# Performance work log

Hardware: AMD Instinct MI355X
Metric: run time of the kernel (lower is better)

The kernel has to match this reference:

```python
import jax, jax.numpy as jnp
import numpy as np


def setup_inputs() -> dict:
    key = jax.random.key(0)
    k1, k2, k3, k4, k5 = jax.random.split(key, 5)
    B, N, M, D = 4096, 2048, 2048, 9
    return {
        "x": jax.random.normal(k1, (B, N), dtype=jnp.float32),
        "eternal_weights": jax.random.normal(k2, (D, N, M), dtype=jnp.float32),
        "eternal_biases": jax.random.normal(k3, (M,), dtype=jnp.float32),
        "classical_weights": jax.random.normal(k4, (N, M), dtype=jnp.float32),
        "classical_biases": jax.random.normal(k5, (M,), dtype=jnp.float32),
    }


def _eternal_probs(eternal_weights, n, m):
    # The gate matrix is cos*I - sin*P + sin*P^T with P the circular shift,
    # so (gate @ s)[i] = cos*s[i] - sin*s[(i+1)%n] + sin*s[(i-1)%n].
    # Vectorize over all m output units at once: state is [m, n].
    state0 = jnp.full((m, n), 1.0 / np.sqrt(n), dtype=eternal_weights.dtype)
    angles = eternal_weights[:, :m, :3]  # [D, m, 3] -- weights[depth, j, 0/1/2]

    def gate(state, angle):  # angle: [m]
        c = jnp.cos(angle)[:, None]
        s = jnp.sin(angle)[:, None]
        return c * state - s * jnp.roll(state, -1, axis=1) + s * jnp.roll(state, 1, axis=1)

    def step(state, ang):  # ang: [m, 3] -- consciousness, intelligence, wisdom
        state = gate(state, ang[:, 0])
        state = gate(state, ang[:, 1])
        state = gate(state, ang[:, 2])
        return state, None

    state, _ = jax.lax.scan(step, state0, angles)
    return jnp.abs(state[:, 0]) ** 2  # [m]


def reference(x, eternal_weights, eternal_biases, classical_weights, classical_biases):
    # eternal_biases exists as a parameter in the original module but is unused in forward.
    n = x.shape[1]
    m = classical_weights.shape[1]
    classical = x @ classical_weights + classical_biases  # [B, m]
    probs = _eternal_probs(eternal_weights, n, m)  # [m], identical for every batch row
    return jnp.tanh(classical + probs[None, :])
```

## Files before the change

### kernel.cpp

```cpp
#include <hip/hip_runtime.h>
#include <hip/hip_fp8.h>
#include <stdint.h>

static constexpr int MM = 4096;
static constexpr int KK = 2048;
static constexpr int NN = 2048;

typedef float floatx16 __attribute__((ext_vector_type(16)));
typedef __bf16 bf16x8 __attribute__((ext_vector_type(8)));
typedef unsigned short u16x8 __attribute__((ext_vector_type(8)));
typedef int intx4 __attribute__((ext_vector_type(4)));
typedef int intx8 __attribute__((ext_vector_type(8)));
typedef unsigned char u8x16 __attribute__((ext_vector_type(16)));

__device__ __forceinline__ unsigned short bf16_rne(float x) {
  union { float f; uint32_t u; } c; c.f = x;
  uint32_t u = c.u;
  u += 0x7fffu + ((u >> 16) & 1u);
  return (unsigned short)(u >> 16);
}
__device__ __forceinline__ float bf16_as_f32(unsigned short h) {
  union { float f; uint32_t u; } c; c.u = ((uint32_t)h) << 16;
  return c.f;
}
__device__ __forceinline__ unsigned char f32_to_e4m3(float x) {
  __hip_fp8_e4m3 q(x);
  return (unsigned char)q.__x;
}
__device__ __forceinline__ float fast_tanh(float x) {
  float e = __expf(2.0f * x);
  return 1.0f - 2.0f / (e + 1.0f);
}


__global__ __launch_bounds__(256) void prepass_kernel(
    const float* __restrict__ x, const float* __restrict__ E,
    const float* __restrict__ W, const float* __restrict__ cb,
    unsigned short* __restrict__ ahi, unsigned char* __restrict__ a8,
    unsigned char* __restrict__ al8,
    unsigned short* __restrict__ bhi, unsigned char* __restrict__ b8,
    unsigned char* __restrict__ bl8, float* __restrict__ bias2) {
  __shared__ float tile[64][65];
  const int blk = blockIdx.x;
  const int tid = threadIdx.x;

  if (blk < 2048) {
    int idx = blk * 256 + tid;
    int row = idx >> 7;
    int u = idx & 127;
    int g = u >> 2;
    int c4 = u & 3;
    const float4* s = (const float4*)(x + (size_t)row * KK + u * 16);
    float v[16];
#pragma unroll
    for (int q = 0; q < 4; q++) {
      float4 t = s[q];
      v[q * 4 + 0] = t.x; v[q * 4 + 1] = t.y; v[q * 4 + 2] = t.z; v[q * 4 + 3] = t.w;
    }
    unsigned short h[16];
    u8x16 f8, fl8;
#pragma unroll
    for (int e = 0; e < 16; e++) {
      h[e] = bf16_rne(v[e]);
      float lo = v[e] - bf16_as_f32(h[e]);
      f8[e] = f32_to_e4m3(v[e]);
      fl8[e] = f32_to_e4m3(lo * 512.0f);
    }
    size_t rb = (size_t)row * KK;
#pragma unroll
    for (int cc = 0; cc < 2; cc++) {
      int c8 = c4 * 2 + cc;
      int phys8 = (c8 + row + (row >> 3)) & 7;
      u16x8 o;
#pragma unroll
      for (int e = 0; e < 8; e++) o[e] = h[cc * 8 + e];
      *(u16x8*)(ahi + rb + g * 64 + phys8 * 8) = o;
    }
    int phys4 = (c4 + (row >> 1) + (row >> 3)) & 3;
    *(u8x16*)(a8 + rb + g * 64 + phys4 * 16) = f8;
    *(u8x16*)(al8 + rb + g * 64 + phys4 * 16) = fl8;
  } else if (blk < 3072) {
    const int wb = blk - 2048;
    const int n0 = (wb & 31) * 64;
    const int k0 = (wb >> 5) * 64;
#pragma unroll
    for (int i = 0; i < 4; i++) {
      int t = tid + i * 256;
      int kr = t >> 4;
      int nc = (t & 15) * 4;
      const float4 vv = *(const float4*)(W + (size_t)(k0 + kr) * NN + n0 + nc);
      tile[nc + 0][kr] = vv.x;
      tile[nc + 1][kr] = vv.y;
      tile[nc + 2][kr] = vv.z;
      tile[nc + 3][kr] = vv.w;
    }
    __syncthreads();
    const int nl = tid >> 2;
    const int q = tid & 3;
    const int n = n0 + nl;
    float v[16];
    unsigned short h[16];
    u8x16 f8, fl8;
#pragma unroll
    for (int e = 0; e < 16; e++) {
      v[e] = tile[nl][q * 16 + e];
      h[e] = bf16_rne(v[e]);
      float lo = v[e] - bf16_as_f32(h[e]);
      f8[e] = f32_to_e4m3(v[e]);
      fl8[e] = f32_to_e4m3(lo * 512.0f);
    }
    size_t rb = (size_t)n * KK + k0;
#pragma unroll
    for (int cc = 0; cc < 2; cc++) {
      int c8 = q * 2 + cc;
      int phys8 = (c8 + n + (n >> 3)) & 7;
      u16x8 o;
#pragma unroll
      for (int e = 0; e < 8; e++) o[e] = h[cc * 8 + e];
      *(u16x8*)(bhi + rb + phys8 * 8) = o;
    }
    int phys4 = (q + (n >> 1) + (n >> 3)) & 3;
    *(u8x16*)(b8 + rb + phys4 * 16) = f8;
    *(u8x16*)(bl8 + rb + phys4 * 16) = fl8;
  } else {
    int i = (blk - 3072) * 256 + tid;
    if (i < NN) {
      float p = 1.0f / 2048.0f;
#pragma unroll
      for (int d = 0; d < 9; d++) {
        const float4 a = *(const float4*)(E + (size_t)d * (2048 * 2048) + (size_t)i * 2048);
        float c0 = cosf(a.x), c1 = cosf(a.y), c2 = cosf(a.z);
        p *= (c0 * c0) * (c1 * c1) * (c2 * c2);
      }
      bias2[i] = cb[i] + p;
    }
  }
}

#define GLL(dst, src)                                                        \
  __builtin_amdgcn_global_load_lds(                                          \
      (const __attribute__((address_space(1))) void*)(src),                  \
      (__attribute__((address_space(3))) void*)(dst), 16, 0, 0)

__global__ __launch_bounds__(256, 2) void gemm_tanh_kernel(
    const unsigned short* __restrict__ Ahi, const unsigned char* __restrict__ A8,
    const unsigned char* __restrict__ Al8,
    const unsigned short* __restrict__ Bhi, const unsigned char* __restrict__ B8,
    const unsigned char* __restrict__ Bl8,
    const float* __restrict__ bias2, float* __restrict__ out) {
  __shared__ __align__(16) unsigned short sAh[128 * 64];
  __shared__ __align__(16) unsigned short sBh[128 * 64];
  __shared__ __align__(16) unsigned char sA8[128 * 64];
  __shared__ __align__(16) unsigned char sAl[128 * 64];
  __shared__ __align__(16) unsigned char sB8[128 * 64];
  __shared__ __align__(16) unsigned char sBl[128 * 64];

  const int tid = threadIdx.x;
  const int lane = tid & 63;
  const int wave = tid >> 6;
  const int wm = (wave >> 1) * 64;
  const int wn = (wave & 1) * 64;

  const int id = blockIdx.x;
  const int cid = id >> 4, lid = id & 15;
  const int bm = ((cid >> 2) * 4 + (lid >> 2)) * 128;
  const int bn = ((cid & 3) * 4 + (lid & 3)) * 128;

  const size_t a16 = (size_t)(bm + (tid >> 3)) * KK + (tid & 7) * 8;
  const size_t b16 = (size_t)(bn + (tid >> 3)) * KK + (tid & 7) * 8;
  const size_t a8b = (size_t)(bm + (tid >> 2)) * KK + (tid & 3) * 16;
  const size_t b8b = (size_t)(bn + (tid >> 2)) * KK + (tid & 3) * 16;
  const int lds16 = tid * 8;
  const int lds8 = tid * 16;

  const int r31 = lane & 31;
  const int half = lane >> 5;

  floatx16 acch[2][2], accc[2][2];
#pragma unroll
  for (int i = 0; i < 2; i++)
#pragma unroll
    for (int j = 0; j < 2; j++)
#pragma unroll
      for (int r = 0; r < 16; r++) { acch[i][j][r] = 0.f; accc[i][j][r] = 0.f; }

  for (int k0 = 0; k0 < KK; k0 += 64) {
#pragma unroll
    for (int p = 0; p < 4; p++) {
      const size_t go = k0 + (size_t)(32 * p) * KK;
      GLL(&sAh[p * 2048 + lds16], Ahi + a16 + go);
      GLL(&sBh[p * 2048 + lds16], Bhi + b16 + go);
    }
#pragma unroll
    for (int p = 0; p < 2; p++) {
      const size_t go = k0 + (size_t)(64 * p) * KK;
      GLL(&sA8[p * 4096 + lds8], A8 + a8b + go);
      GLL(&sAl[p * 4096 + lds8], Al8 + a8b + go);
      GLL(&sB8[p * 4096 + lds8], B8 + b8b + go);
      GLL(&sBl[p * 4096 + lds8], Bl8 + b8b + go);
    }
    __syncthreads();

#pragma unroll
    for (int s = 0; s < 4; s++) {
      const int c8 = s * 2 + half;
      bf16x8 fa[2], fb[2];
#pragma unroll
      for (int t = 0; t < 2; t++) {
        int rowA = wm + t * 32 + r31;
        int ao = rowA * 64 + ((c8 + rowA + (rowA >> 3)) & 7) * 8;
        fa[t] = *(const bf16x8*)(&sAh[ao]);
        int rowB = wn + t * 32 + r31;
        int bo = rowB * 64 + ((c8 + rowB + (rowB >> 3)) & 7) * 8;
        fb[t] = *(const bf16x8*)(&sBh[bo]);
      }
#pragma unroll
      for (int i = 0; i < 2; i++)
#pragma unroll
        for (int j = 0; j < 2; j++)
          acch[i][j] = __builtin_amdgcn_mfma_f32_32x32x16_bf16(fa[i], fb[j], acch[i][j], 0, 0, 0);
    }

    {
      intx8 fal[2], fb8[2];
#pragma unroll
      for (int t = 0; t < 2; t++) {
        int rowA = wm + t * 32 + r31;
        int rowB = wn + t * 32 + r31;
#pragma unroll
        for (int cc = 0; cc < 2; cc++) {
          int c4 = half * 2 + cc;
          int pa = (c4 + (rowA >> 1) + (rowA >> 3)) & 3;
          ((intx4*)&fal[t])[cc] = *(const intx4*)(&sAl[rowA * 64 + pa * 16]);
          int pb = (c4 + (rowB >> 1) + (rowB >> 3)) & 3;
          ((intx4*)&fb8[t])[cc] = *(const intx4*)(&sB8[rowB * 64 + pb * 16]);
        }
      }
#pragma unroll
      for (int i = 0; i < 2; i++)
#pragma unroll
        for (int j = 0; j < 2; j++)
          accc[i][j] = __builtin_amdgcn_mfma_scale_f32_32x32x64_f8f6f4(
              fal[i], fb8[j], accc[i][j], 0, 0, 0, 0x7f7f7f7f, 0, 0x7f7f7f7f);

      intx8 fa8[2], fbl[2];
#pragma unroll
      for (int t = 0; t < 2; t++) {
        int rowA = wm + t * 32 + r31;
        int rowB = wn + t * 32 + r31;
#pragma unroll
        for (int cc = 0; cc < 2; cc++) {
          int c4 = half * 2 + cc;
          int pa = (c4 + (rowA >> 1) + (rowA >> 3)) & 3;
          ((intx4*)&fa8[t])[cc] = *(const intx4*)(&sA8[rowA * 64 + pa * 16]);
          int pb = (c4 + (rowB >> 1) + (rowB >> 3)) & 3;
          ((intx4*)&fbl[t])[cc] = *(const intx4*)(&sBl[rowB * 64 + pb * 16]);
        }
      }
#pragma unroll
      for (int i = 0; i < 2; i++)
#pragma unroll
        for (int j = 0; j < 2; j++)
          accc[i][j] = __builtin_amdgcn_mfma_scale_f32_32x32x64_f8f6f4(
              fa8[i], fbl[j], accc[i][j], 0, 0, 0, 0x7f7f7f7f, 0, 0x7f7f7f7f);
    }
    __syncthreads();
  }

#pragma unroll
  for (int j = 0; j < 2; j++) {
    int col = bn + wn + j * 32 + r31;
    float b2 = bias2[col];
#pragma unroll
    for (int i = 0; i < 2; i++) {
      int row0 = bm + wm + i * 32 + 4 * half;
#pragma unroll
      for (int r = 0; r < 16; r++) {
        int row = row0 + (r & 3) + 8 * (r >> 2);
        float val = acch[i][j][r] + accc[i][j][r] * (1.0f / 512.0f) + b2;
        __builtin_nontemporal_store(fast_tanh(val), &out[(size_t)row * NN + col]);
      }
    }
  }
}

__global__ __launch_bounds__(256) void fallback_gemm(
    const float* __restrict__ x, const float* __restrict__ E,
    const float* __restrict__ W, const float* __restrict__ cb,
    float* __restrict__ out) {
  __shared__ float sA[16][16];
  __shared__ float sB[16][17];
  __shared__ float sbias[16];
  const int tx = threadIdx.x, ty = threadIdx.y;
  const int row = blockIdx.y * 16 + ty;
  const int col = blockIdx.x * 16 + tx;
  if (ty == 0) {
    float p = 1.0f / 2048.0f;
    for (int d = 0; d < 9; d++) {
      const float* a = E + (size_t)d * (2048 * 2048) + (size_t)col * 2048;
      for (int t = 0; t < 3; t++) { float c = cosf(a[t]); p *= c * c; }
    }
    sbias[tx] = p + cb[col];
  }
  float acc = 0.f;
  for (int k0 = 0; k0 < KK; k0 += 16) {
    __syncthreads();
    sA[ty][tx] = x[(size_t)row * KK + k0 + tx];
    sB[ty][tx] = W[(size_t)(k0 + ty) * NN + col];
    __syncthreads();
#pragma unroll
    for (int kk = 0; kk < 16; kk++) acc += sA[ty][kk] * sB[kk][tx];
  }
  out[(size_t)row * NN + col] = tanhf(acc + sbias[tx]);
}

extern "C" void kernel_launch(void* const* d_in, const int* in_sizes, int n_in,
                              void* d_out, int out_size, void* d_ws, size_t ws_size,
                              hipStream_t stream) {
  const float* x  = (const float*)d_in[0];
  const float* E  = (const float*)d_in[1];
  const float* W  = (const float*)d_in[3];
  const float* cb = (const float*)d_in[4];
  float* out = (float*)d_out;

  const size_t MB = 1024 * 1024;
  const size_t need = 48 * MB + NN * sizeof(float);
  if (ws_size < need) {
    fallback_gemm<<<dim3(NN / 16, MM / 16), dim3(16, 16), 0, stream>>>(x, E, W, cb, out);
    return;
  }

  char* ws = (char*)d_ws;
  unsigned short* Ahi = (unsigned short*)(ws);
  unsigned short* Bhi = (unsigned short*)(ws + 16 * MB);
  unsigned char* A8   = (unsigned char*)(ws + 24 * MB);
  unsigned char* Al8  = (unsigned char*)(ws + 32 * MB);
  unsigned char* B8   = (unsigned char*)(ws + 40 * MB);
  unsigned char* Bl8  = (unsigned char*)(ws + 44 * MB);
  float* bias2 = (float*)(ws + 48 * MB);

  prepass_kernel<<<dim3(3080), dim3(256), 0, stream>>>(
      x, E, W, cb, Ahi, A8, Al8, Bhi, B8, Bl8, bias2);
  gemm_tanh_kernel<<<dim3(512), dim3(256), 0, stream>>>(
      Ahi, A8, Al8, Bhi, B8, Bl8, bias2, out);
}
```

Baseline: 304.0 us.

## Derive fp8 operands in-register from bf16 and double-buffer bf16 tiles

Stops writing and reloading separate fp8 copies of A and B. The fp8 high parts are now built in registers from the bf16 fragments already loaded, which cuts prepass stores, workspace size and GEMM global/LDS traffic. The 1/512 rescale of the correction term moves into the MFMA scale exponent, so the two accumulator sets merge into one. The bf16 tiles are double-buffered with explicit vmcnt waits and split barriers so loads overlap compute. This adds conversion ALU work inside the main loop and changes the rounding path for the fp8 high part (bf16 then fp8 instead of fp32 then fp8).

New measurement: 308.3 us. Within noise of the previous version (+1.4%).

```diff
diff --git a/kernel.cpp b/kernel.cpp
--- a/kernel.cpp
+++ b/kernel.cpp
@@ -31,15 +31,20 @@
   float e = __expf(2.0f * x);
   return 1.0f - 2.0f / (e + 1.0f);
 }
+__device__ __forceinline__ float bflo(unsigned int w) {
+  union { float f; unsigned u; } c; c.u = w << 16; return c.f;
+}
+__device__ __forceinline__ float bfhi(unsigned int w) {
+  union { float f; unsigned u; } c; c.u = w & 0xffff0000u; return c.f;
+}
 
 
 __global__ __launch_bounds__(256) void prepass_kernel(
     const float* __restrict__ x, const float* __restrict__ E,
     const float* __restrict__ W, const float* __restrict__ cb,
-    unsigned short* __restrict__ ahi, unsigned char* __restrict__ a8,
-    unsigned char* __restrict__ al8,
-    unsigned short* __restrict__ bhi, unsigned char* __restrict__ b8,
-    unsigned char* __restrict__ bl8, float* __restrict__ bias2) {
+    unsigned short* __restrict__ ahi, unsigned char* __restrict__ al8,
+    unsigned short* __restrict__ bhi, unsigned char* __restrict__ bl8,
+    float* __restrict__ bias2) {
   __shared__ float tile[64][65];
   const int blk = blockIdx.x;
   const int tid = threadIdx.x;
@@ -49,36 +54,39 @@
     int row = idx >> 7;
     int u = idx & 127;
     int g = u >> 2;
-    int c4 = u & 3;
+    int q = u & 3;
     const float4* s = (const float4*)(x + (size_t)row * KK + u * 16);
     float v[16];
 #pragma unroll
-    for (int q = 0; q < 4; q++) {
-      float4 t = s[q];
-      v[q * 4 + 0] = t.x; v[q * 4 + 1] = t.y; v[q * 4 + 2] = t.z; v[q * 4 + 3] = t.w;
+    for (int p = 0; p < 4; p++) {
+      float4 t = s[p];
+      v[p * 4 + 0] = t.x; v[p * 4 + 1] = t.y; v[p * 4 + 2] = t.z; v[p * 4 + 3] = t.w;
     }
     unsigned short h[16];
-    u8x16 f8, fl8;
+    union { unsigned char b[16]; unsigned long long d[2]; } loq;
 #pragma unroll
     for (int e = 0; e < 16; e++) {
       h[e] = bf16_rne(v[e]);
       float lo = v[e] - bf16_as_f32(h[e]);
-      f8[e] = f32_to_e4m3(v[e]);
-      fl8[e] = f32_to_e4m3(lo * 512.0f);
+      loq.b[e] = f32_to_e4m3(lo * 512.0f);
     }
     size_t rb = (size_t)row * KK;
 #pragma unroll
     for (int cc = 0; cc < 2; cc++) {
-      int c8 = c4 * 2 + cc;
+      int c8 = q * 2 + cc;
       int phys8 = (c8 + row + (row >> 3)) & 7;
       u16x8 o;
 #pragma unroll
       for (int e = 0; e < 8; e++) o[e] = h[cc * 8 + e];
       *(u16x8*)(ahi + rb + g * 64 + phys8 * 8) = o;
     }
-    int phys4 = (c4 + (row >> 1) + (row >> 3)) & 3;
-    *(u8x16*)(a8 + rb + g * 64 + phys4 * 16) = f8;
-    *(u8x16*)(al8 + rb + g * 64 + phys4 * 16) = fl8;
+    {
+      int sw = (row & 3) + ((row >> 2) & 3);
+      int cA = (q >> 1) * 2;
+      char* lb = (char*)al8 + rb + g * 64;
+      *(unsigned long long*)(lb + (((cA + 0) + sw) & 3) * 16 + (q & 1) * 8) = loq.d[0];
+      *(unsigned long long*)(lb + (((cA + 1) + sw) & 3) * 16 + (q & 1) * 8) = loq.d[1];
+    }
   } else if (blk < 3072) {
     const int wb = blk - 2048;
     const int n0 = (wb & 31) * 64;
@@ -100,14 +108,13 @@
     const int n = n0 + nl;
     float v[16];
     unsigned short h[16];
-    u8x16 f8, fl8;
+    union { unsigned char b[16]; unsigned long long d[2]; } loq;
 #pragma unroll
     for (int e = 0; e < 16; e++) {
       v[e] = tile[nl][q * 16 + e];
       h[e] = bf16_rne(v[e]);
       float lo = v[e] - bf16_as_f32(h[e]);
-      f8[e] = f32_to_e4m3(v[e]);
-      fl8[e] = f32_to_e4m3(lo * 512.0f);
+      loq.b[e] = f32_to_e4m3(lo * 512.0f);
     }
     size_t rb = (size_t)n * KK + k0;
 #pragma unroll
@@ -119,9 +126,13 @@
       for (int e = 0; e < 8; e++) o[e] = h[cc * 8 + e];
       *(u16x8*)(bhi + rb + phys8 * 8) = o;
     }
-    int phys4 = (q + (n >> 1) + (n >> 3)) & 3;
-    *(u8x16*)(b8 + rb + phys4 * 16) = f8;
-    *(u8x16*)(bl8 + rb + phys4 * 16) = fl8;
+    {
+      int sw = (n & 3) + ((n >> 2) & 3);
+      int cA = (q >> 1) * 2;
+      char* lb = (char*)bl8 + rb;
+      *(unsigned long long*)(lb + (((cA + 0) + sw) & 3) * 16 + (q & 1) * 8) = loq.d[0];
+      *(unsigned long long*)(lb + (((cA + 1) + sw) & 3) * 16 + (q & 1) * 8) = loq.d[1];
+    }
   } else {
     int i = (blk - 3072) * 256 + tid;
     if (i < NN) {
@@ -143,16 +154,12 @@
       (__attribute__((address_space(3))) void*)(dst), 16, 0, 0)
 
 __global__ __launch_bounds__(256, 2) void gemm_tanh_kernel(
-    const unsigned short* __restrict__ Ahi, const unsigned char* __restrict__ A8,
-    const unsigned char* __restrict__ Al8,
-    const unsigned short* __restrict__ Bhi, const unsigned char* __restrict__ B8,
-    const unsigned char* __restrict__ Bl8,
+    const unsigned short* __restrict__ Ahi, const unsigned char* __restrict__ Al8,
+    const unsigned short* __restrict__ Bhi, const unsigned char* __restrict__ Bl8,
     const float* __restrict__ bias2, float* __restrict__ out) {
-  __shared__ __align__(16) unsigned short sAh[128 * 64];
-  __shared__ __align__(16) unsigned short sBh[128 * 64];
-  __shared__ __align__(16) unsigned char sA8[128 * 64];
+  __shared__ __align__(16) unsigned short sAh[2][128 * 64];
+  __shared__ __align__(16) unsigned short sBh[2][128 * 64];
   __shared__ __align__(16) unsigned char sAl[128 * 64];
-  __shared__ __align__(16) unsigned char sB8[128 * 64];
   __shared__ __align__(16) unsigned char sBl[128 * 64];
 
   const int tid = threadIdx.x;
@@ -176,31 +183,44 @@
   const int r31 = lane & 31;
   const int half = lane >> 5;
 
-  floatx16 acch[2][2], accc[2][2];
+  floatx16 acc[2][2];
 #pragma unroll
   for (int i = 0; i < 2; i++)
 #pragma unroll
     for (int j = 0; j < 2; j++)
 #pragma unroll
-      for (int r = 0; r < 16; r++) { acch[i][j][r] = 0.f; accc[i][j][r] = 0.f; }
-
-  for (int k0 = 0; k0 < KK; k0 += 64) {
+      for (int r = 0; r < 16; r++) acc[i][j][r] = 0.f;
+
+#pragma unroll
+  for (int p = 0; p < 4; p++) {
+    GLL(&sAh[0][p * 2048 + lds16], Ahi + a16 + (size_t)(32 * p) * KK);
+    GLL(&sBh[0][p * 2048 + lds16], Bhi + b16 + (size_t)(32 * p) * KK);
+  }
+
+  for (int kt = 0; kt < 32; ++kt) {
+    const int k0 = kt * 64;
+    const int cur = kt & 1;
+    const int nxt = cur ^ 1;
+
+    __builtin_amdgcn_s_barrier();
+    __builtin_amdgcn_sched_barrier(0);
+#pragma unroll
+    for (int p = 0; p < 2; p++) {
+      GLL(&sAl[p * 4096 + lds8], Al8 + a8b + (size_t)k0 + (size_t)(64 * p) * KK);
+      GLL(&sBl[p * 4096 + lds8], Bl8 + b8b + (size_t)k0 + (size_t)(64 * p) * KK);
+    }
+    const size_t kn = (kt < 31) ? (size_t)(k0 + 64) : 0;
 #pragma unroll
     for (int p = 0; p < 4; p++) {
-      const size_t go = k0 + (size_t)(32 * p) * KK;
-      GLL(&sAh[p * 2048 + lds16], Ahi + a16 + go);
-      GLL(&sBh[p * 2048 + lds16], Bhi + b16 + go);
-    }
-#pragma unroll
-    for (int p = 0; p < 2; p++) {
-      const size_t go = k0 + (size_t)(64 * p) * KK;
-      GLL(&sA8[p * 4096 + lds8], A8 + a8b + go);
-      GLL(&sAl[p * 4096 + lds8], Al8 + a8b + go);
-      GLL(&sB8[p * 4096 + lds8], B8 + b8b + go);
-      GLL(&sBl[p * 4096 + lds8], Bl8 + b8b + go);
-    }
-    __syncthreads();
-
+      GLL(&sAh[nxt][p * 2048 + lds16], Ahi + a16 + kn + (size_t)(32 * p) * KK);
+      GLL(&sBh[nxt][p * 2048 + lds16], Bhi + b16 + kn + (size_t)(32 * p) * KK);
+    }
+    asm volatile("s_waitcnt vmcnt(12)" ::: "memory");
+    __builtin_amdgcn_sched_barrier(0);
+    __builtin_amdgcn_s_barrier();
+    __builtin_amdgcn_sched_barrier(0);
+
+    intx8 fa8[2], fb8[2];
 #pragma unroll
     for (int s = 0; s < 4; s++) {
       const int c8 = s * 2 + half;
@@ -209,62 +229,62 @@
       for (int t = 0; t < 2; t++) {
         int rowA = wm + t * 32 + r31;
         int ao = rowA * 64 + ((c8 + rowA + (rowA >> 3)) & 7) * 8;
-        fa[t] = *(const bf16x8*)(&sAh[ao]);
+        fa[t] = *(const bf16x8*)(&sAh[cur][ao]);
         int rowB = wn + t * 32 + r31;
         int bo = rowB * 64 + ((c8 + rowB + (rowB >> 3)) & 7) * 8;
-        fb[t] = *(const bf16x8*)(&sBh[bo]);
+        fb[t] = *(const bf16x8*)(&sBh[cur][bo]);
       }
 #pragma unroll
       for (int i = 0; i < 2; i++)
 #pragma unroll
         for (int j = 0; j < 2; j++)
-          acch[i][j] = __builtin_amdgcn_mfma_f32_32x32x16_bf16(fa[i], fb[j], acch[i][j], 0, 0, 0);
-    }
-
-    {
-      intx8 fal[2], fb8[2];
+          acc[i][j] = __builtin_amdgcn_mfma_f32_32x32x16_bf16(fa[i], fb[j], acc[i][j], 0, 0, 0);
 #pragma unroll
       for (int t = 0; t < 2; t++) {
-        int rowA = wm + t * 32 + r31;
-        int rowB = wn + t * 32 + r31;
-#pragma unroll
-        for (int cc = 0; cc < 2; cc++) {
-          int c4 = half * 2 + cc;
-          int pa = (c4 + (rowA >> 1) + (rowA >> 3)) & 3;
-          ((intx4*)&fal[t])[cc] = *(const intx4*)(&sAl[rowA * 64 + pa * 16]);
-          int pb = (c4 + (rowB >> 1) + (rowB >> 3)) & 3;
-          ((intx4*)&fb8[t])[cc] = *(const intx4*)(&sB8[rowB * 64 + pb * 16]);
-        }
+        uint4 ua = *(const uint4*)&fa[t];
+        int d0 = __builtin_amdgcn_cvt_pk_fp8_f32(bflo(ua.x), bfhi(ua.x), 0, false);
+        d0 = __builtin_amdgcn_cvt_pk_fp8_f32(bflo(ua.y), bfhi(ua.y), d0, true);
+        int d1 = __builtin_amdgcn_cvt_pk_fp8_f32(bflo(ua.z), bfhi(ua.z), 0, false);
+        d1 = __builtin_amdgcn_cvt_pk_fp8_f32(bflo(ua.w), bfhi(ua.w), d1, true);
+        fa8[t][2 * s] = d0; fa8[t][2 * s + 1] = d1;
+        uint4 ub = *(const uint4*)&fb[t];
+        int e0 = __builtin_amdgcn_cvt_pk_fp8_f32(bflo(ub.x), bfhi(ub.x), 0, false);
+        e0 = __builtin_amdgcn_cvt_pk_fp8_f32(bflo(ub.y), bfhi(ub.y), e0, true);
+        int e1 = __builtin_amdgcn_cvt_pk_fp8_f32(bflo(ub.z), bfhi(ub.z), 0, false);
+        e1 = __builtin_amdgcn_cvt_pk_fp8_f32(bflo(ub.w), bfhi(ub.w), e1, true);
+        fb8[t][2 * s] = e0; fb8[t][2 * s + 1] = e1;
       }
-#pragma unroll
-      for (int i = 0; i < 2; i++)
-#pragma unroll
-        for (int j = 0; j < 2; j++)
-          accc[i][j] = __builtin_amdgcn_mfma_scale_f32_32x32x64_f8f6f4(
-              fal[i], fb8[j], accc[i][j], 0, 0, 0, 0x7f7f7f7f, 0, 0x7f7f7f7f);
-
-      intx8 fa8[2], fbl[2];
-#pragma unroll
-      for (int t = 0; t < 2; t++) {
-        int rowA = wm + t * 32 + r31;
-        int rowB = wn + t * 32 + r31;
-#pragma unroll
-        for (int cc = 0; cc < 2; cc++) {
-          int c4 = half * 2 + cc;
-          int pa = (c4 + (rowA >> 1) + (rowA >> 3)) & 3;
-          ((intx4*)&fa8[t])[cc] = *(const intx4*)(&sA8[rowA * 64 + pa * 16]);
-          int pb = (c4 + (rowB >> 1) + (rowB >> 3)) & 3;
-          ((intx4*)&fbl[t])[cc] = *(const intx4*)(&sBl[rowB * 64 + pb * 16]);
-        }
-      }
-#pragma unroll
-      for (int i = 0; i < 2; i++)
-#pragma unroll
-        for (int j = 0; j < 2; j++)
-          accc[i][j] = __builtin_amdgcn_mfma_scale_f32_32x32x64_f8f6f4(
-              fa8[i], fbl[j], accc[i][j], 0, 0, 0, 0x7f7f7f7f, 0, 0x7f7f7f7f);
-    }
-    __syncthreads();
+    }
+
+    asm volatile("s_waitcnt vmcnt(8)" ::: "memory");
+    __builtin_amdgcn_sched_barrier(0);
+    __builtin_amdgcn_s_barrier();
+    __builtin_amdgcn_sched_barrier(0);
+
+    intx8 fal[2], fbl[2];
+#pragma unroll
+    for (int t = 0; t < 2; t++) {
+      int rowA = wm + t * 32 + r31;
+      int swA = (rowA & 3) + ((rowA >> 2) & 3);
+      ((intx4*)&fal[t])[0] = *(const intx4*)(&sAl[rowA * 64 + ((half + swA) & 3) * 16]);
+      ((intx4*)&fal[t])[1] = *(const intx4*)(&sAl[rowA * 64 + ((2 + half + swA) & 3) * 16]);
+      int rowB = wn + t * 32 + r31;
+      int swB = (rowB & 3) + ((rowB >> 2) & 3);
+      ((intx4*)&fbl[t])[0] = *(const intx4*)(&sBl[rowB * 64 + ((half + swB) & 3) * 16]);
+      ((intx4*)&fbl[t])[1] = *(const intx4*)(&sBl[rowB * 64 + ((2 + half + swB) & 3) * 16]);
+    }
+#pragma unroll
+    for (int i = 0; i < 2; i++)
+#pragma unroll
+      for (int j = 0; j < 2; j++)
+        acc[i][j] = __builtin_amdgcn_mfma_scale_f32_32x32x64_f8f6f4(
+            fal[i], fb8[j], acc[i][j], 0, 0, 0, 0x76767676, 0, 0x7f7f7f7f);
+#pragma unroll
+    for (int i = 0; i < 2; i++)
+#pragma unroll
+      for (int j = 0; j < 2; j++)
+        acc[i][j] = __builtin_amdgcn_mfma_scale_f32_32x32x64_f8f6f4(
+            fa8[i], fbl[j], acc[i][j], 0, 0, 0, 0x7f7f7f7f, 0, 0x76767676);
   }
 
 #pragma unroll
@@ -277,7 +297,7 @@
 #pragma unroll
       for (int r = 0; r < 16; r++) {
         int row = row0 + (r & 3) + 8 * (r >> 2);
-        float val = acch[i][j][r] + accc[i][j][r] * (1.0f / 512.0f) + b2;
+        float val = acc[i][j][r] + b2;
         __builtin_nontemporal_store(fast_tanh(val), &out[(size_t)row * NN + col]);
       }
     }
@@ -324,7 +344,7 @@
   float* out = (float*)d_out;
 
   const size_t MB = 1024 * 1024;
-  const size_t need = 48 * MB + NN * sizeof(float);
+  const size_t need = 36 * MB + NN * sizeof(float);
   if (ws_size < need) {
     fallback_gemm<<<dim3(NN / 16, MM / 16), dim3(16, 16), 0, stream>>>(x, E, W, cb, out);
     return;
@@ -333,14 +353,12 @@
   char* ws = (char*)d_ws;
   unsigned short* Ahi = (unsigned short*)(ws);
   unsigned short* Bhi = (unsigned short*)(ws + 16 * MB);
-  unsigned char* A8   = (unsigned char*)(ws + 24 * MB);
-  unsigned char* Al8  = (unsigned char*)(ws + 32 * MB);
-  unsigned char* B8   = (unsigned char*)(ws + 40 * MB);
-  unsigned char* Bl8  = (unsigned char*)(ws + 44 * MB);
-  float* bias2 = (float*)(ws + 48 * MB);
+  unsigned char* Al8  = (unsigned char*)(ws + 24 * MB);
+  unsigned char* Bl8  = (unsigned char*)(ws + 32 * MB);
+  float* bias2 = (float*)(ws + 36 * MB);
 
   prepass_kernel<<<dim3(3080), dim3(256), 0, stream>>>(
-      x, E, W, cb, Ahi, A8, Al8, Bhi, B8, Bl8, bias2);
+      x, E, W, cb, Ahi, Al8, Bhi, Bl8, bias2);
   gemm_tanh_kernel<<<dim3(512), dim3(256), 0, stream>>>(
-      Ahi, A8, Al8, Bhi, B8, Bl8, bias2, out);
-}
+      Ahi, Al8, Bhi, Bl8, bias2, out);
+}
```
